# Optimization experiments

Hardware: AMD Instinct MI355X
Metric: run time of the kernel (lower is better)

## Reference

```python
import jax, jax.numpy as jnp
import numpy as np

B, N, C = 8, 1025, 768
NUM_HEADS = 12
HEAD_DIM = C // NUM_HEADS  # 64, also depthwise-conv channel count
HW = (32, 32)              # N = 1 + 32*32 (cls token)
SCALE = HEAD_DIM ** -0.5
VALUE_MASK_FILL = -10000.0
LN_EPS = 1e-5


def setup_inputs() -> dict:
    key = jax.random.key(0)
    ks = jax.random.split(key, 12)
    s = 0.02
    inp = {
        "x": jax.random.normal(ks[0], (B, N, C), jnp.float32),
        "mask": jax.random.bernoulli(ks[1], 0.9, (B, N)),
        "Wq": jax.random.normal(ks[2], (C, C), jnp.float32) * s,
        "Wk": jax.random.normal(ks[3], (C, C), jnp.float32) * s,
        "Wv": jax.random.normal(ks[4], (C, C), jnp.float32) * s,
        "pool_q_w": jax.random.normal(ks[5], (HEAD_DIM, 1, 3, 3), jnp.float32) * s,
        "pool_k_w": jax.random.normal(ks[6], (HEAD_DIM, 1, 3, 3), jnp.float32) * s,
        "pool_v_w": jax.random.normal(ks[7], (HEAD_DIM, 1, 3, 3), jnp.float32) * s,
        "gq": jnp.ones((HEAD_DIM,), jnp.float32),
        "bq": jnp.zeros((HEAD_DIM,), jnp.float32),
        "gk": jnp.ones((HEAD_DIM,), jnp.float32),
        "bk": jnp.zeros((HEAD_DIM,), jnp.float32),
        "gv": jnp.ones((HEAD_DIM,), jnp.float32),
        "bv": jnp.zeros((HEAD_DIM,), jnp.float32),
        "Wp": jax.random.normal(ks[8], (C, C), jnp.float32) * s,
        "bp": jnp.zeros((C,), jnp.float32),
    }
    return inp


def _layernorm(t, g, b):
    m = jnp.mean(t, axis=-1, keepdims=True)
    v = jnp.var(t, axis=-1, keepdims=True)
    return (t - m) * jax.lax.rsqrt(v + LN_EPS) * g + b


def _depthwise(t, w):
    # t: [BH, D, H, W], w: [D, 1, 3, 3] depthwise, stride 1, SAME padding
    return jax.lax.conv_general_dilated(
        t, w, window_strides=(1, 1), padding="SAME",
        dimension_numbers=("NCHW", "OIHW", "NCHW"),
        feature_group_count=t.shape[1])


def _attn_pool(t, w, g, b):
    # t: [B, H, N, D] with leading cls token; pool spatial tokens, norm after
    Bb, Hh, Nn, D = t.shape
    cls_tok, spat = t[:, :, :1], t[:, :, 1:]
    Hs, Ws = HW
    spat = spat.reshape(Bb * Hh, Hs, Ws, D).transpose(0, 3, 1, 2)
    spat = _depthwise(spat, w)
    spat = spat.reshape(Bb, Hh, D, Hs * Ws).transpose(0, 1, 3, 2)
    t = jnp.concatenate([cls_tok, spat], axis=2)
    return _layernorm(t, g, b)


def reference(x, mask, Wq, Wk, Wv, pool_q_w, pool_k_w, pool_v_w,
              gq, bq, gk, bk, gv, bv, Wp, bp):
    Bb, Nn, Cc = x.shape
    # QKV projections (no bias), split heads -> [B, H, N, D]
    q = (x @ Wq.T).reshape(Bb, Nn, NUM_HEADS, HEAD_DIM).transpose(0, 2, 1, 3)
    k = (x @ Wk.T).reshape(Bb, Nn, NUM_HEADS, HEAD_DIM).transpose(0, 2, 1, 3)
    v = (x @ Wv.T).reshape(Bb, Nn, NUM_HEADS, HEAD_DIM).transpose(0, 2, 1, 3)
    q = _attn_pool(q, pool_q_w, gq, bq)
    k = _attn_pool(k, pool_k_w, gk, bk)
    v = _attn_pool(v, pool_v_w, gv, bv)
    attn = jnp.einsum("bhqd,bhkd->bhqk", q, k) * SCALE
    # mask: [B, N] bool; broadcast as (B,1,N,1), False -> value_mask_fill
    attn = jnp.where(mask[:, None, :, None], attn, VALUE_MASK_FILL)
    attn = jax.nn.softmax(attn, axis=-1)
    attn_origin = attn
    out = jnp.einsum("bhqk,bhkd->bhqd", attn, v)
    # residual pooling, skipping the cls token
    out = jnp.concatenate([out[:, :, :1], out[:, :, 1:] + q[:, :, 1:]], axis=2)
    out = out.transpose(0, 2, 1, 3).reshape(Bb, Nn, Cc)
    out = out @ Wp.T + bp
    return out, attn_origin
```

## Files before the change

### kernel.cpp

```cpp
#include <hip/hip_runtime.h>
#include <hip/hip_bf16.h>
#include <cstdint>
#include <cstddef>

typedef unsigned short u16;
typedef __attribute__((ext_vector_type(8))) short bf16x8;
typedef __attribute__((ext_vector_type(4))) float f32x4;

#define MFMA16(a,b,c) __builtin_amdgcn_mfma_f32_16x16x32_bf16(a,b,c,0,0,0)
#define GLL16(gp, lp) __builtin_amdgcn_global_load_lds( \
    (const __attribute__((address_space(1))) void*)(gp), \
    (__attribute__((address_space(3))) void*)(lp), 16, 0, 0)

static constexpr int kB = 8, kH = 12, kN = 1025, kC = 768, kD = 64;
static constexpr int kBH = kB*kH;
static constexpr int kNP = 1056;
static constexpr int kM  = kB*kN;
static constexpr float kScale = 0.125f;

__device__ __forceinline__ u16 f2b(float f){
  unsigned u = __builtin_bit_cast(unsigned, f);
  u = (u + 0x7fffu + ((u>>16)&1u)) >> 16;
  return (u16)u;
}
__device__ __forceinline__ float b2f(u16 s){
  unsigned u = ((unsigned)s)<<16;
  return __builtin_bit_cast(float, u);
}
__device__ __forceinline__ unsigned pkbf(float a, float b){
  unsigned r;
  asm("v_cvt_pk_bf16_f32 %0, %1, %2" : "=v"(r) : "v"(a), "v"(b));
  return r;
}
__device__ __forceinline__ int xcd_swz(int orig, int nwg){
  int q = nwg>>3, r = nwg&7;
  int xcd = orig&7, idx = orig>>3;
  return (xcd<r ? xcd*(q+1) : r*(q+1)+(xcd-r)*q) + idx;
}

__global__ __launch_bounds__(256) void k_prep(const float4* __restrict__ x,
    const float* __restrict__ w0, const float* __restrict__ w1,
    const float* __restrict__ w2, const float* __restrict__ w3,
    const unsigned char* __restrict__ m,
    u16* __restrict__ xb, u16* __restrict__ wb, int* __restrict__ maskn){
  __shared__ int cnt;
  const int bid = blockIdx.x;
  if (bid < 6150){
    int i = bid*256 + threadIdx.x;
    float4 v = x[i];
    ushort4 o; o.x=f2b(v.x); o.y=f2b(v.y); o.z=f2b(v.z); o.w=f2b(v.w);
    *reinterpret_cast<ushort4*>(xb + (size_t)i*4) = o;
  } else if (bid < 8454){
    int j = (bid-6150)*256 + threadIdx.x;
    int sel = j/147456, i = j - sel*147456;
    const float* ws[4] = {w0,w1,w2,w3};
    float4 v = reinterpret_cast<const float4*>(ws[sel])[i];
    ushort4 o; o.x=f2b(v.x); o.y=f2b(v.y); o.z=f2b(v.z); o.w=f2b(v.w);
    *reinterpret_cast<ushort4*>(wb + (size_t)sel*589824 + (size_t)i*4) = o;
  } else {
    if (threadIdx.x==0) cnt = 0;
    __syncthreads();
    int local = 0;
    for (int i=threadIdx.x; i<1024; i+=256) local += (m[i]!=0);
    atomicAdd(&cnt, local);
    __syncthreads();
    bool b8 = (cnt > 512);
    int lb = bid - 8454;
    for (int i = lb*256 + threadIdx.x; i < kM; i += 32*256){
      int v = b8 ? (m[i]!=0) : (reinterpret_cast<const int*>(m)[i] != 0);
      maskn[i] = v;
    }
  }
}

template<int MODE>
__global__ __launch_bounds__(256) void k_gemm128(const u16* __restrict__ A,
      const u16* __restrict__ wb, const float* __restrict__ bias,
      u16* __restrict__ outb, float* __restrict__ outf){
  __shared__ union SM {
    struct { u16 a[128*32]; u16 b[128*32]; } s;
    u16 c2[64*136];
  } sm;
  constexpr int NB = (MODE==0) ? 18 : 6;
  const int wg = xcd_swz(blockIdx.x, gridDim.x);
  const int m0 = (wg / NB)*128;
  const int N0 = (wg % NB)*128;
  const int sel = (MODE==0) ? (N0/768) : 3;
  const int jb  = (MODE==0) ? (N0%768) : N0;
  const u16* W = wb + (size_t)sel*589824;
  const int t = threadIdx.x;
  const int wave = t>>6, lane = t&63;
  const int g = lane>>4, cl = lane&15;
  const int wr2 = (wave>>1)*64, wc2 = (wave&1)*64;

  const int cid0 = wave*64 + lane;
  const int cid1 = cid0 + 256;
  const int ar0 = m0 + (cid0>>2) < kM ? m0 + (cid0>>2) : kM-1;
  const int ar1 = m0 + (cid1>>2) < kM ? m0 + (cid1>>2) : kM-1;
  const int ac0 = (cid0&3)<<3, ac1 = (cid1&3)<<3;
  const int br0 = jb + (cid0>>2), br1 = jb + (cid1>>2);
  u16* lA0 = &sm.s.a[(wave*64)*8];
  u16* lA1 = &sm.s.a[(256 + wave*64)*8];
  u16* lB0 = &sm.s.b[(wave*64)*8];
  u16* lB1 = &sm.s.b[(256 + wave*64)*8];

  f32x4 acc[4][4];
  #pragma unroll
  for (int i=0;i<4;i++)
    #pragma unroll
    for (int j=0;j<4;j++) acc[i][j] = (f32x4){0.f,0.f,0.f,0.f};

  for (int k0=0; k0<768; k0+=32){
    __syncthreads();
    GLL16(A + (size_t)ar0*768 + k0 + ac0, lA0);
    GLL16(A + (size_t)ar1*768 + k0 + ac1, lA1);
    GLL16(W + (size_t)br0*768 + k0 + ac0, lB0);
    GLL16(W + (size_t)br1*768 + k0 + ac1, lB1);
    __syncthreads();
    bf16x8 af[4], bfg[4];
    #pragma unroll
    for (int fm=0; fm<4; fm++)
      af[fm] = *reinterpret_cast<const bf16x8*>(&sm.s.a[(wr2+fm*16+cl)*32 + g*8]);
    #pragma unroll
    for (int fn=0; fn<4; fn++)
      bfg[fn] = *reinterpret_cast<const bf16x8*>(&sm.s.b[(wc2+fn*16+cl)*32 + g*8]);
    #pragma unroll
    for (int fm=0; fm<4; fm++)
      #pragma unroll
      for (int fn=0; fn<4; fn++)
        acc[fm][fn] = MFMA16(af[fm], bfg[fn], acc[fm][fn]);
  }

  if (MODE==0){
    #pragma unroll
    for (int ph=0; ph<2; ++ph){
      __syncthreads();
      if ((wave>>1) == ph){
        #pragma unroll
        for (int fm=0; fm<4; fm++)
          #pragma unroll
          for (int fn=0; fn<4; fn++)
            #pragma unroll
            for (int i=0;i<4;i++){
              int r = fm*16 + g*4 + i;
              int c = wc2 + fn*16 + cl;
              sm.c2[r*136 + c] = f2b(acc[fm][fn][i]);
            }
      }
      __syncthreads();
      #pragma unroll
      for (int it=0; it<4; it++){
        int cid = t + it*256;
        int r = cid >> 4, cc = (cid & 15) * 8;
        int gm = m0 + ph*64 + r;
        if (gm < kM){
          *reinterpret_cast<uint4*>(&outb[(size_t)gm*2304 + N0 + cc]) =
              *reinterpret_cast<const uint4*>(&sm.c2[r*136 + cc]);
        }
      }
    }
  } else {
    #pragma unroll
    for (int fm=0; fm<4; fm++)
      #pragma unroll
      for (int fn=0; fn<4; fn++)
        #pragma unroll
        for (int i=0;i<4;i++){
          int gm = m0 + wr2 + fm*16 + g*4 + i;
          if (gm >= kM) continue;
          int gc = jb + wc2 + fn*16 + cl;
          outf[(size_t)gm*768 + gc] = acc[fm][fn][i] + bias[gc];
        }
  }
}

__global__ __launch_bounds__(256) void k_pool3(const u16* __restrict__ qkvmat,
    const float* __restrict__ wq, const float* __restrict__ wk, const float* __restrict__ wv,
    const float* __restrict__ gq, const float* __restrict__ bq,
    const float* __restrict__ gk, const float* __restrict__ bk,
    const float* __restrict__ gv, const float* __restrict__ bv,
    u16* __restrict__ Qp, u16* __restrict__ Kp, u16* __restrict__ Vt){
  __shared__ u16 vt[64][72];
  const int which = blockIdx.y;
  const float* w9 = (which==0)?wq:(which==1)?wk:wv;
  const float* gg = (which==0)?gq:(which==1)?gk:gv;
  const float* bb2= (which==0)?bq:(which==1)?bk:bv;
  u16* out = (which==0)?Qp:(which==1)?Kp:Vt;

  const int wave = threadIdx.x>>6, d = threadIdx.x&63;
  const int wg  = xcd_swz(blockIdx.x, 96*17);
  const int nb  = wg % 17;
  const int bh  = wg / 17;
  const int b = bh/12, h = bh - b*12;
  const int np0 = nb*64;
  const u16* base = qkvmat + ((size_t)b*1025)*2304 + which*768 + h*64;

  float wreg[9];
  #pragma unroll
  for (int j=0;j<9;j++) wreg[j] = w9[d*9+j];
  const float gd = gg[d], bd = bb2[d];

  for (int iter=0; iter<16; ++iter){
    const int np = np0 + iter*4 + wave;
    float v = 0.f;
    if (np < kN){
      if (np == 0){
        v = b2f(base[d]);
      } else {
        int y = (np-1)>>5, x = (np-1)&31;
        #pragma unroll
        for (int ky=0; ky<3; ky++){
          int yy = y+ky-1;
          if (yy<0 || yy>31) continue;
          #pragma unroll
          for (int kx=0; kx<3; kx++){
            int xx = x+kx-1;
            if (xx<0 || xx>31) continue;
            v += wreg[ky*3+kx] * b2f(base[(size_t)(1+yy*32+xx)*2304 + d]);
          }
        }
      }
      float s = v, s2 = v*v;
      #pragma unroll
      for (int off=1; off<64; off<<=1){ s += __shfl_xor(s, off); s2 += __shfl_xor(s2, off); }
      float mean = s*(1.f/64.f);
      float var  = s2*(1.f/64.f) - mean*mean;
      v = (v-mean)*rsqrtf(var+1e-5f)*gd + bd;
    }
    if (which==2) vt[d][iter*4+wave] = f2b(v);
    else if (np < kNP) out[((size_t)bh*kNP + np)*kD + d] = f2b(v);
  }

  if (which==2){
    __syncthreads();
    const int dr = threadIdx.x>>2, seg = threadIdx.x&3;
    if (np0 + seg*16 < kNP){
      u16* dst = Vt + ((size_t)bh*kD + dr)*kNP + np0 + seg*16;
      *reinterpret_cast<uint4*>(dst)     = *reinterpret_cast<const uint4*>(&vt[dr][seg*16]);
      *reinterpret_cast<uint4*>(dst + 8) = *reinterpret_cast<const uint4*>(&vt[dr][seg*16+8]);
    }
  }
}

__global__ __launch_bounds__(256) void k_attn(const u16* __restrict__ Qp, const u16* __restrict__ Kp,
    const u16* __restrict__ Vt, const int* __restrict__ maskn,
    float* __restrict__ attn_out, u16* __restrict__ ctx){
  constexpr int LDE = 1064;
  __shared__ u16 E[16*LDE];
  __shared__ float Lrow[16];
  __shared__ float Linv[16];
  const int wave = threadIdx.x>>6, lane = threadIdx.x&63;
  const int xcd  = blockIdx.x & 7;
  const int slot = blockIdx.x >> 3;
  const int bh = xcd*12 + slot/65;
  const int qt = slot%65;
  const int b  = bh / 12, h = bh - b*12;
  const int qbase = qt*16;
  const int g = lane>>4, cl = lane&15;

  if (threadIdx.x < 16) Lrow[threadIdx.x] = 0.f;
  __syncthreads();

  const u16* qrow = Qp + ((size_t)bh*kNP + (qbase + cl))*kD + g*8;
  bf16x8 aq0 = *reinterpret_cast<const bf16x8*>(qrow);
  bf16x8 aq1 = *reinterpret_cast<const bf16x8*>(qrow + 32);

  const int qi_l = qbase + cl;
  const float mqc = (qi_l < kN && maskn[b*kN + qi_l] != 0) ? kScale : 0.f;

  const u16* kb = Kp + (size_t)bh*kNP*kD;
  float rsum = 0.f;
  u16* erow = &E[cl*LDE];
  #pragma unroll 2
  for (int kt=wave; kt<32; kt+=4){
    const int ktb = kt*32;
    const u16* kr = kb + (size_t)(ktb+cl)*kD + g*8;
    bf16x8 b00 = *reinterpret_cast<const bf16x8*>(kr);
    bf16x8 b01 = *reinterpret_cast<const bf16x8*>(kr+32);
    bf16x8 b10 = *reinterpret_cast<const bf16x8*>(kr+1024);
    bf16x8 b11 = *reinterpret_cast<const bf16x8*>(kr+1024+32);
    f32x4 s0 = {0.f,0.f,0.f,0.f}, s1 = {0.f,0.f,0.f,0.f};
    __builtin_amdgcn_s_setprio(1);
    s0 = MFMA16(b00,aq0,s0); s0 = MFMA16(b01,aq1,s0);
    s1 = MFMA16(b10,aq0,s1); s1 = MFMA16(b11,aq1,s1);
    __builtin_amdgcn_s_setprio(0);
    float e0 = __expf(s0[0]*mqc), e1 = __expf(s0[1]*mqc);
    float e2 = __expf(s0[2]*mqc), e3 = __expf(s0[3]*mqc);
    float f0 = __expf(s1[0]*mqc), f1 = __expf(s1[1]*mqc);
    float f2 = __expf(s1[2]*mqc), f3 = __expf(s1[3]*mqc);
    rsum += ((e0+e1)+(e2+e3)) + ((f0+f1)+(f2+f3));
    uint2 w0v = { pkbf(e0,e1), pkbf(e2,e3) };
    uint2 w1v = { pkbf(f0,f1), pkbf(f2,f3) };
    *reinterpret_cast<uint2*>(&erow[ktb + 4*g])      = w0v;
    *reinterpret_cast<uint2*>(&erow[ktb + 16 + 4*g]) = w1v;
  }
  if (wave == 0){
    const int ktb = 1024;
    const u16* kr = kb + (size_t)(ktb+cl)*kD + g*8;
    bf16x8 b00 = *reinterpret_cast<const bf16x8*>(kr);
    bf16x8 b01 = *reinterpret_cast<const bf16x8*>(kr+32);
    f32x4 s0 = {0.f,0.f,0.f,0.f};
    s0 = MFMA16(b00,aq0,s0); s0 = MFMA16(b01,aq1,s0);
    float e0 = (g==0) ? __expf(s0[0]*mqc) : 0.f;
    rsum += e0;
    uint2 w0v = { pkbf(e0,0.f), 0u };
    uint2 zz  = { 0u, 0u };
    *reinterpret_cast<uint2*>(&erow[ktb + 4*g])      = w0v;
    *reinterpret_cast<uint2*>(&erow[ktb + 16 + 4*g]) = zz;
  }
  rsum += __shfl_xor(rsum, 16);
  rsum += __shfl_xor(rsum, 32);
  if (lane < 16) atomicAdd(&Lrow[cl], rsum);
  __syncthreads();
  if (threadIdx.x < 16) Linv[threadIdx.x] = 1.f/Lrow[threadIdx.x];
  __syncthreads();

  {
    size_t S = (size_t)bh*kN*kN + (size_t)qbase*kN;
    float* tp = attn_out + S;
    int rows = kN - qbase; if (rows > 16) rows = 16;
    int T = rows*kN;
    int head = (int)((4 - (S & 3)) & 3);
    int body4 = (T - head) >> 2;
    int tail = T - head - body4*4;
    int t = threadIdx.x;
    if (t < head){
      int e = t;
      unsigned row = ((unsigned)(e*16369))>>24;
      int col = e - (int)row*kN;
      tp[e] = b2f(E[row*LDE+col]) * Linv[row];
    }
    if (t < tail){
      int e = head + body4*4 + t;
      unsigned row = ((unsigned)(e*16369))>>24;
      int col = e - (int)row*kN;
      tp[e] = b2f(E[row*LDE+col]) * Linv[row];
    }
    for (int idx = t; idx < body4; idx += 256){
      int e = head + idx*4;
      unsigned row0 = ((unsigned)(e*16369))>>24;
      unsigned row3 = ((unsigned)((e+3)*16369))>>24;
      float4 vv;
      if (row0 == row3){
        int col = e - (int)row0*kN;
        const u16* ep = &E[row0*LDE + col];
        float li = Linv[row0];
        vv.x = b2f(ep[0])*li; vv.y = b2f(ep[1])*li;
        vv.z = b2f(ep[2])*li; vv.w = b2f(ep[3])*li;
      } else {
        float tmp[4];
        #pragma unroll
        for (int j=0;j<4;j++){
          int ee = e+j;
          unsigned row = ((unsigned)(ee*16369))>>24;
          int col = ee - (int)row*kN;
          tmp[j] = b2f(E[row*LDE+col]) * Linv[row];
        }
        vv.x=tmp[0]; vv.y=tmp[1]; vv.z=tmp[2]; vv.w=tmp[3];
      }
      *reinterpret_cast<float4*>(tp + e) = vv;
    }
  }

  const int d0 = wave*16;
  f32x4 oacc = (f32x4){0.f,0.f,0.f,0.f};
  const u16* vb = Vt + ((size_t)bh*kD + d0 + cl)*kNP;
  for (int kt0=0; kt0<32; kt0+=4){
    bf16x8 pa[4], vv[4];
    #pragma unroll
    for (int j=0;j<4;j++){
      const int ko = (kt0+j)*32 + g*8;
      pa[j] = *reinterpret_cast<const bf16x8*>(&E[cl*LDE + ko]);
      vv[j] = *reinterpret_cast<const bf16x8*>(vb + ko);
    }
    __builtin_amdgcn_s_setprio(1);
    #pragma unroll
    for (int j=0;j<4;j++) oacc = MFMA16(pa[j], vv[j], oacc);
    __builtin_amdgcn_s_setprio(0);
  }
  {
    const int ko = 32*32 + g*8;
    bf16x8 pa = *reinterpret_cast<const bf16x8*>(&E[cl*LDE + ko]);
    bf16x8 vv = *reinterpret_cast<const bf16x8*>(vb + ko);
    oacc = MFMA16(pa, vv, oacc);
  }
  #pragma unroll
  for (int i=0;i<4;i++){
    int row = g*4+i, qi = qbase+row;
    if (qi < kN){
      float val = oacc[i] * Linv[row];
      int dd = d0 + cl;
      if (qi >= 1) val += b2f(Qp[((size_t)bh*kNP + qi)*kD + dd]);
      ctx[((size_t)(b*kN + qi))*kC + h*kD + dd] = f2b(val);
    }
  }
}

extern "C" void kernel_launch(void* const* d_in, const int* in_sizes, int n_in,
                              void* d_out, int out_size, void* d_ws, size_t ws_size,
                              hipStream_t stream) {
  const float* x    = (const float*)d_in[0];
  const void*  msk  = d_in[1];
  const float* Wq   = (const float*)d_in[2];
  const float* Wk   = (const float*)d_in[3];
  const float* Wv   = (const float*)d_in[4];
  const float* pw_q = (const float*)d_in[5];
  const float* pw_k = (const float*)d_in[6];
  const float* pw_v = (const float*)d_in[7];
  const float* gq   = (const float*)d_in[8];
  const float* bq   = (const float*)d_in[9];
  const float* gk   = (const float*)d_in[10];
  const float* bk   = (const float*)d_in[11];
  const float* gv   = (const float*)d_in[12];
  const float* bv   = (const float*)d_in[13];
  const float* Wp   = (const float*)d_in[14];
  const float* bp   = (const float*)d_in[15];

  char* ws = (char*)d_ws;
  u16* xb     = (u16*)(ws + 0);
  u16* wb     = (u16*)(ws + 12595200);
  int* maskn  = (int*)(ws + 17313792);
  u16* qkvmat = (u16*)(ws + 17346816);
  u16* Qp     = (u16*)(ws + 55132416);
  u16* Kp     = (u16*)(ws + 68108544);
  u16* Vt     = (u16*)(ws + 81084672);
  u16* ctx    = (u16*)(ws + 17346816);

  float* out1 = (float*)d_out;
  float* attn = out1 + (size_t)kM*kC;

  k_prep<<<8486, 256, 0, stream>>>(reinterpret_cast<const float4*>(x),
                                   Wq, Wk, Wv, Wp, (const unsigned char*)msk,
                                   xb, wb, maskn);
  k_gemm128<0><<<65*18, 256, 0, stream>>>(xb, wb, nullptr, qkvmat, nullptr);
  k_pool3<<<dim3(96*17,3), 256, 0, stream>>>(qkvmat, pw_q, pw_k, pw_v,
                                             gq, bq, gk, bk, gv, bv, Qp, Kp, Vt);
  k_attn<<<96*65, 256, 0, stream>>>(Qp, Kp, Vt, maskn, attn, ctx);
  k_gemm128<1><<<65*6, 256, 0, stream>>>(ctx, wb, bp, nullptr, out1);
}
```

Baseline: 406.8 us.

## Split attention block into PV-MFMA waves and concurrent attn-prob writer waves

The attention kernel block grows from 256 to 512 threads. The QK^T/exp phase is spread over 8 waves, and after normalization the first 4 waves do the P·V MFMA and context write while the other 4 waves stream the normalized probability matrix to global memory at the same time. Before, one set of waves ran these two phases one after the other, so the large fp32 attn store and the PV compute were serialized. The risk is that launch_bounds(512,8) can limit registers, and the PV loop loses its 4-way unrolled loads and setprio.

```diff
diff --git a/kernel.cpp b/kernel.cpp
--- a/kernel.cpp
+++ b/kernel.cpp
@@ -242,7 +242,7 @@
   }
 }
 
-__global__ __launch_bounds__(256) void k_attn(const u16* __restrict__ Qp, const u16* __restrict__ Kp,
+__global__ __launch_bounds__(512, 8) void k_attn(const u16* __restrict__ Qp, const u16* __restrict__ Kp,
     const u16* __restrict__ Vt, const int* __restrict__ maskn,
     float* __restrict__ attn_out, u16* __restrict__ ctx){
   constexpr int LDE = 1064;
@@ -271,8 +271,8 @@
   const u16* kb = Kp + (size_t)bh*kNP*kD;
   float rsum = 0.f;
   u16* erow = &E[cl*LDE];
-  #pragma unroll 2
-  for (int kt=wave; kt<32; kt+=4){
+  #pragma unroll 1
+  for (int kt=wave; kt<32; kt+=8){
     const int ktb = kt*32;
     const u16* kr = kb + (size_t)(ktb+cl)*kD + g*8;
     bf16x8 b00 = *reinterpret_cast<const bf16x8*>(kr);
@@ -315,7 +315,28 @@
   if (threadIdx.x < 16) Linv[threadIdx.x] = 1.f/Lrow[threadIdx.x];
   __syncthreads();
 
-  {
+  if (wave < 4){
+    const int d0 = wave*16;
+    f32x4 oacc = (f32x4){0.f,0.f,0.f,0.f};
+    const u16* vb = Vt + ((size_t)bh*kD + d0 + cl)*kNP;
+    for (int kt=0; kt<33; kt++){
+      const int ko = kt*32 + g*8;
+      bf16x8 pa = *reinterpret_cast<const bf16x8*>(&E[cl*LDE + ko]);
+      bf16x8 vv = *reinterpret_cast<const bf16x8*>(vb + ko);
+      oacc = MFMA16(pa, vv, oacc);
+    }
+    #pragma unroll
+    for (int i=0;i<4;i++){
+      int row = g*4+i, qi = qbase+row;
+      if (qi < kN){
+        float val = oacc[i] * Linv[row];
+        int dd = d0 + cl;
+        if (qi >= 1) val += b2f(Qp[((size_t)bh*kNP + qi)*kD + dd]);
+        ctx[((size_t)(b*kN + qi))*kC + h*kD + dd] = f2b(val);
+      }
+    }
+  } else {
+    const int t2 = threadIdx.x - 256;
     size_t S = (size_t)bh*kN*kN + (size_t)qbase*kN;
     float* tp = attn_out + S;
     int rows = kN - qbase; if (rows > 16) rows = 16;
@@ -323,20 +344,19 @@
     int head = (int)((4 - (S & 3)) & 3);
     int body4 = (T - head) >> 2;
     int tail = T - head - body4*4;
-    int t = threadIdx.x;
-    if (t < head){
-      int e = t;
+    if (t2 < head){
+      int e = t2;
       unsigned row = ((unsigned)(e*16369))>>24;
       int col = e - (int)row*kN;
       tp[e] = b2f(E[row*LDE+col]) * Linv[row];
     }
-    if (t < tail){
-      int e = head + body4*4 + t;
+    if (t2 < tail){
+      int e = head + body4*4 + t2;
       unsigned row = ((unsigned)(e*16369))>>24;
       int col = e - (int)row*kN;
       tp[e] = b2f(E[row*LDE+col]) * Linv[row];
     }
-    for (int idx = t; idx < body4; idx += 256){
+    for (int idx = t2; idx < body4; idx += 256){
       int e = head + idx*4;
       unsigned row0 = ((unsigned)(e*16369))>>24;
       unsigned row3 = ((unsigned)((e+3)*16369))>>24;
@@ -361,39 +381,6 @@
       *reinterpret_cast<float4*>(tp + e) = vv;
     }
   }
-
-  const int d0 = wave*16;
-  f32x4 oacc = (f32x4){0.f,0.f,0.f,0.f};
-  const u16* vb = Vt + ((size_t)bh*kD + d0 + cl)*kNP;
-  for (int kt0=0; kt0<32; kt0+=4){
-    bf16x8 pa[4], vv[4];
-    #pragma unroll
-    for (int j=0;j<4;j++){
-      const int ko = (kt0+j)*32 + g*8;
-      pa[j] = *reinterpret_cast<const bf16x8*>(&E[cl*LDE + ko]);
-      vv[j] = *reinterpret_cast<const bf16x8*>(vb + ko);
-    }
-    __builtin_amdgcn_s_setprio(1);
-    #pragma unroll
-    for (int j=0;j<4;j++) oacc = MFMA16(pa[j], vv[j], oacc);
-    __builtin_amdgcn_s_setprio(0);
-  }
-  {
-    const int ko = 32*32 + g*8;
-    bf16x8 pa = *reinterpret_cast<const bf16x8*>(&E[cl*LDE + ko]);
-    bf16x8 vv = *reinterpret_cast<const bf16x8*>(vb + ko);
-    oacc = MFMA16(pa, vv, oacc);
-  }
-  #pragma unroll
-  for (int i=0;i<4;i++){
-    int row = g*4+i, qi = qbase+row;
-    if (qi < kN){
-      float val = oacc[i] * Linv[row];
-      int dd = d0 + cl;
-      if (qi >= 1) val += b2f(Qp[((size_t)bh*kNP + qi)*kD + dd]);
-      ctx[((size_t)(b*kN + qi))*kC + h*kD + dd] = f2b(val);
-    }
-  }
 }
 
 extern "C" void kernel_launch(void* const* d_in, const int* in_sizes, int n_in,
@@ -435,6 +422,6 @@
   k_gemm128<0><<<65*18, 256, 0, stream>>>(xb, wb, nullptr, qkvmat, nullptr);
   k_pool3<<<dim3(96*17,3), 256, 0, stream>>>(qkvmat, pw_q, pw_k, pw_v,
                                              gq, bq, gk, bk, gv, bv, Qp, Kp, Vt);
-  k_attn<<<96*65, 256, 0, stream>>>(Qp, Kp, Vt, maskn, attn, ctx);
+  k_attn<<<96*65, 512, 0, stream>>>(Qp, Kp, Vt, maskn, attn, ctx);
   k_gemm128<1><<<65*6, 256, 0, stream>>>(ctx, wb, bp, nullptr, out1);
 }
```

After: 395.9 us. -2.7%, faster.
